# Kernel optimization log

Measured on AMD Instinct MI355X. Metric: run time of the kernel, lower is better.

The kernel has to match this reference:

```python
import jax, jax.numpy as jnp
import numpy as np

B, T_DEC, T_ENC = 64, 128, 256
D_IN, D_ENC, H = 256, 512, 512


def setup_inputs() -> dict:
    key = jax.random.key(0)
    ks = jax.random.split(key, 8)
    s = 0.05  # keras 'uniform' init is small; keep params modest
    return {
        "inputs": jax.random.normal(ks[0], (B, T_DEC, D_IN), jnp.float32),
        "context_mat": jax.random.normal(ks[1], (B, T_ENC, D_ENC), jnp.float32),
        "att_w1": jax.random.uniform(ks[2], (H + D_ENC, D_ENC), jnp.float32, -s, s),
        "att_w2": jax.random.uniform(ks[3], (D_ENC, 1), jnp.float32, -s, s),
        "Wx": jax.random.uniform(ks[4], (D_IN + D_ENC, 3 * H), jnp.float32, -s, s),
        "Wh": jax.random.uniform(ks[5], (H, 3 * H), jnp.float32, -s, s),
        "b": jnp.zeros((3 * H,), jnp.float32),
    }


def reference(inputs, context_mat, att_w1, att_w2, Wx, Wh, b):
    # inputs: [B, T_dec, d_in]; context_mat: [B, T_enc, d_enc]
    Bn, Te, De = context_mat.shape
    Hn = Wh.shape[0]

    def step(h, x_t):
        # --- Bahdanau-style attention (concat -> relu(MLP) -> softmax) ---
        key_rep = jnp.broadcast_to(h[:, None, :], (Bn, Te, Hn))
        concated = jnp.concatenate([key_rep, context_mat], axis=-1)  # [B,Te,H+De]
        energies = jax.nn.relu(
            jnp.einsum('bte,eo->bto', concated @ att_w1, att_w2)[..., 0]
        )  # [B, Te]
        att = jax.nn.softmax(energies, axis=-1)
        ctx = jnp.einsum('bt,btd->bd', att, context_mat)  # [B, De]
        # --- GRU cell (reset_after=False, classic Keras) ---
        xin = jnp.concatenate([x_t, ctx], axis=-1)  # [B, d_in+De]
        gx = xin @ Wx + b  # [B, 3H]
        xz, xr, xh = gx[:, :Hn], gx, gx  # slices below
        xz = gx[:, :Hn]
        xr = gx[:, Hn:2 * Hn]
        xh = gx[:, 2 * Hn:]
        z = jax.nn.sigmoid(xz + h @ Wh[:, :Hn])
        r = jax.nn.sigmoid(xr + h @ Wh[:, Hn:2 * Hn])
        hh = jnp.tanh(xh + (r * h) @ Wh[:, 2 * Hn:])
        h_new = z * h + (1.0 - z) * hh
        return h_new, h_new

    h0 = jnp.zeros((Bn, Hn), inputs.dtype)
    xs = jnp.swapaxes(inputs, 0, 1)  # [T_dec, B, d_in]
    _, outs = jax.lax.scan(step, h0, xs)  # [T_dec, B, H]
    return jnp.swapaxes(outs, 0, 1)  # [B, T_dec, H]
```

## Files before the change

kernel.cpp:

```cpp
#include <hip/hip_runtime.h>

#define NBLK  256
#define NTHR  384
#define TDEC  128
#define TENC  256
#define DIN   256
#define DENC  512
#define HHH   512
#define NG    1536
#define KTOT  1280
#define NK4   320
#define ASTR  516
#define ASTR4 129

#define FLAGS_BYTES (128*3*16*16)
#define OFF_U     24576
#define OFF_ECTX  25600
#define OFF_HG    41984
#define OFF_CTXG  74752
#define OFF_RHG   107520
#define OFF_WP    140288
#define WP_ELEMS  (16*NK4*96*4)

__device__ __forceinline__ float wave_sum(float v) {
#pragma unroll
    for (int o = 32; o; o >>= 1) v += __shfl_down(v, o, 64);
    return v;
}
__device__ __forceinline__ float wave_max(float v) {
#pragma unroll
    for (int o = 32; o; o >>= 1) v = fmaxf(v, __shfl_down(v, o, 64));
    return v;
}
__device__ __forceinline__ void stA(float* p, float v) {
    __hip_atomic_store(p, v, __ATOMIC_RELAXED, __HIP_MEMORY_SCOPE_AGENT);
}
__device__ __forceinline__ float2 ldA2(float* p) {
    double d = __hip_atomic_load((double*)p, __ATOMIC_RELAXED, __HIP_MEMORY_SCOPE_AGENT);
    return *(float2*)&d;
}
__device__ __forceinline__ void drain_stores() {
    asm volatile("s_waitcnt vmcnt(0)" ::: "memory");
}
__device__ __forceinline__ void setflag(unsigned char* p) {
    __hip_atomic_store(p, (unsigned char)1, __ATOMIC_RELAXED, __HIP_MEMORY_SCOPE_AGENT);
}
__device__ __forceinline__ void waitflags16(unsigned* f) {
    for (;;) {
        unsigned a0 = __hip_atomic_load(f + 0, __ATOMIC_RELAXED, __HIP_MEMORY_SCOPE_AGENT);
        unsigned a1 = __hip_atomic_load(f + 1, __ATOMIC_RELAXED, __HIP_MEMORY_SCOPE_AGENT);
        unsigned a2 = __hip_atomic_load(f + 2, __ATOMIC_RELAXED, __HIP_MEMORY_SCOPE_AGENT);
        unsigned a3 = __hip_atomic_load(f + 3, __ATOMIC_RELAXED, __HIP_MEMORY_SCOPE_AGENT);
        if ((a0 & a1 & a2 & a3) == 0x01010101u) return;
        __builtin_amdgcn_s_sleep(2);
    }
}
__device__ __forceinline__ float blo(unsigned u) { return __uint_as_float(u << 16); }
__device__ __forceinline__ float bhi(unsigned u) { return __uint_as_float(u & 0xffff0000u); }
__device__ __forceinline__ unsigned short f2bf(float f) {
    unsigned u = __float_as_uint(f);
    u += 0x7fffu + ((u >> 16) & 1u);
    return (unsigned short)(u >> 16);
}

template<bool BF>
__device__ __forceinline__ float4 dotq(const void* wp, int cg, int kcol,
                                       int k4lo, int k4hi, const float* abase,
                                       int aoff, float4 acc) {
    if (BF) {
        const uint2* w = (const uint2*)wp + (size_t)cg*NK4*96 + kcol;
#pragma unroll 4
        for (int k4 = k4lo; k4 < k4hi; ++k4) {
            uint2 uu = w[(size_t)k4 * 96];
            float wx = blo(uu.x), wy = bhi(uu.x), wz = blo(uu.y), ww = bhi(uu.y);
            const float* ao = abase + (k4 - aoff)*4;
            float4 A0 = *(const float4*)(ao + 0*ASTR);
            float4 A1 = *(const float4*)(ao + 1*ASTR);
            float4 A2 = *(const float4*)(ao + 2*ASTR);
            float4 A3 = *(const float4*)(ao + 3*ASTR);
            acc.x = fmaf(wx, A0.x, acc.x); acc.x = fmaf(wy, A0.y, acc.x);
            acc.x = fmaf(wz, A0.z, acc.x); acc.x = fmaf(ww, A0.w, acc.x);
            acc.y = fmaf(wx, A1.x, acc.y); acc.y = fmaf(wy, A1.y, acc.y);
            acc.y = fmaf(wz, A1.z, acc.y); acc.y = fmaf(ww, A1.w, acc.y);
            acc.z = fmaf(wx, A2.x, acc.z); acc.z = fmaf(wy, A2.y, acc.z);
            acc.z = fmaf(wz, A2.z, acc.z); acc.z = fmaf(ww, A2.w, acc.z);
            acc.w = fmaf(wx, A3.x, acc.w); acc.w = fmaf(wy, A3.y, acc.w);
            acc.w = fmaf(wz, A3.z, acc.w); acc.w = fmaf(ww, A3.w, acc.w);
        }
    } else {
        const float4* w = (const float4*)wp + (size_t)cg*NK4*96 + kcol;
#pragma unroll 4
        for (int k4 = k4lo; k4 < k4hi; ++k4) {
            float4 wv = w[(size_t)k4 * 96];
            const float* ao = abase + (k4 - aoff)*4;
            float4 A0 = *(const float4*)(ao + 0*ASTR);
            float4 A1 = *(const float4*)(ao + 1*ASTR);
            float4 A2 = *(const float4*)(ao + 2*ASTR);
            float4 A3 = *(const float4*)(ao + 3*ASTR);
            acc.x = fmaf(wv.x, A0.x, acc.x); acc.x = fmaf(wv.y, A0.y, acc.x);
            acc.x = fmaf(wv.z, A0.z, acc.x); acc.x = fmaf(wv.w, A0.w, acc.x);
            acc.y = fmaf(wv.x, A1.x, acc.y); acc.y = fmaf(wv.y, A1.y, acc.y);
            acc.y = fmaf(wv.z, A1.z, acc.y); acc.y = fmaf(wv.w, A1.w, acc.y);
            acc.z = fmaf(wv.x, A2.x, acc.z); acc.z = fmaf(wv.y, A2.y, acc.z);
            acc.z = fmaf(wv.z, A2.z, acc.z); acc.z = fmaf(wv.w, A2.w, acc.z);
            acc.w = fmaf(wv.x, A3.x, acc.w); acc.w = fmaf(wv.y, A3.y, acc.w);
            acc.w = fmaf(wv.z, A3.z, acc.w); acc.w = fmaf(wv.w, A3.w, acc.w);
        }
    }
    return acc;
}

__global__ void k_u(const float* __restrict__ w1, const float* __restrict__ w2,
                    float* __restrict__ u) {
    int e = blockIdx.x;
    int lane = threadIdx.x;
    float p = 0.f;
#pragma unroll
    for (int k = lane; k < DENC; k += 64) p += w1[e*DENC + k] * w2[k];
    p = wave_sum(p);
    if (lane == 0) u[e] = p;
}

__global__ void k_ectx(const float* __restrict__ C, const float* __restrict__ u,
                       float* __restrict__ ectx) {
    int r = blockIdx.x*4 + (threadIdx.x >> 6);
    int lane = threadIdx.x & 63;
    const float* row = C + (size_t)r*DENC;
    const float* vc  = u + HHH;
    float p = 0.f;
#pragma unroll
    for (int k = 0; k < DENC/64; ++k) p += row[lane + k*64] * vc[lane + k*64];
    p = wave_sum(p);
    if (lane == 0) ectx[r] = p;
}

template<bool BF>
__global__ void k_wpack(const float* __restrict__ Wx, const float* __restrict__ Wh,
                        void* __restrict__ wp) {
    int id = blockIdx.x*256 + threadIdx.x;
    int e = id & 3;
    int q = id >> 2;
    int col = q % 96;
    q /= 96;
    int k4 = q % NK4;
    int cg = q / NK4;
    int k = k4*4 + e;
    int j = (col >> 5)*512 + cg*32 + (col & 31);
    float v = (k < 768) ? Wx[(size_t)k*NG + j] : Wh[(size_t)(k-768)*NG + j];
    if (BF) ((unsigned short*)wp)[id] = f2bf(v);
    else    ((float*)wp)[id] = v;
}

template<bool BF>
__launch_bounds__(NTHR, 1)
__global__ void decoder(const float* __restrict__ inp, const float* __restrict__ C,
                        const float* __restrict__ bias, const void* __restrict__ wpv,
                        const float* __restrict__ u, float* __restrict__ ectx_g,
                        float* __restrict__ out, float* __restrict__ ws) {
    unsigned char* fl = (unsigned char*)ws;
    float* hG   = ws + OFF_HG;
    float* ctxG = ws + OFF_CTXG;
    float* rhG  = ws + OFF_RHG;

    const int tid  = threadIdx.x;
    const int w    = tid >> 6;
    const int blk  = blockIdx.x;
    const int bg   = blk >> 4;
    const int cg   = blk & 15;
    const int b_att = blk >> 2;
    const int ds    = blk & 3;
    const int bl_att = b_att & 3;
    const int ks   = tid / 96;
    const int kcol = tid - ks*96;
    const int sub  = kcol >> 5;
    const int q32k = kcol & 31;
    const int jpk  = cg*32 + q32k;

    __shared__ float sh_C[TENC*128];
    __shared__ __align__(16) float sh_st[4*ASTR];
    __shared__ __align__(16) float sh_h[4*ASTR];
    __shared__ __align__(16) float sh_part[1536];
    __shared__ float sh_att[TENC];
    __shared__ float sh_ectx[TENC];
    __shared__ __align__(16) float sh_u[512];
    __shared__ float sh_z[128];
    __shared__ float sh_cred[2][128];
    __shared__ float sh_red[4];
    __shared__ float sh_hdp[2];

    const float4* u4 = (const float4*)sh_u;

    for (int i = tid; i < TENC*128; i += NTHR)
        sh_C[i] = C[((size_t)b_att*TENC + (i >> 7))*DENC + ds*128 + (i & 127)];
    if (tid < TENC) sh_ectx[tid] = ectx_g[b_att*TENC + tid];
    if (tid < 128) ((float4*)sh_u)[tid] = ((const float4*)(u))[tid];
    const float bias_c = bias[sub*512 + jpk];

    for (int t = 0; t < TDEC; ++t) {
        __syncthreads();
        if (tid < 256) {
            int bb = tid >> 6, k4i = tid & 63;
            *(float4*)&sh_st[bb*ASTR + k4i*4] =
                *(const float4*)&inp[((size_t)(bg*4 + bb)*TDEC + t)*DIN + k4i*4];
        }
        __syncthreads();

        float4 acc = make_float4(ks == 0 ? bias_c : 0.f, ks == 0 ? bias_c : 0.f,
                                 ks == 0 ? bias_c : 0.f, ks == 0 ? bias_c : 0.f);
        acc = dotq<BF>(wpv, cg, kcol, ks*16, ks*16 + 16, sh_st, 0, acc);

        if (t > 0) {
            if (tid == 0) waitflags16((unsigned*)(fl + ((((t-1)*3 + 2)*16 + bg) << 4)));
            __syncthreads();
        }
        if (t > 0) {
            for (int i = tid; i < 1024; i += NTHR) {
                int bb = i >> 8, j2 = (i & 255)*2;
                float2 f = ldA2(&hG[(size_t)(bg*4 + bb)*HHH + j2]);
                *(float2*)&sh_h[bb*ASTR + j2] = f;
            }
        } else {
            for (int i = tid; i < 1024; i += NTHR) {
                int bb = i >> 8, j2 = (i & 255)*2;
                *(float2*)&sh_h[bb*ASTR + j2] = make_float2(0.f, 0.f);
            }
        }
        __syncthreads();

        if (tid < 128) {
            float4 uu = u4[tid];
            float4 hh = ((const float4*)(sh_h + bl_att*ASTR))[tid];
            float p = uu.x*hh.x + uu.y*hh.y + uu.z*hh.z + uu.w*hh.w;
            p = wave_sum(p);
            if ((tid & 63) == 0) sh_hdp[w] = p;
        }
        __syncthreads();
        const float hd = sh_hdp[0] + sh_hdp[1];

        if (tid < TENC) {
            float e = fmaxf(hd + sh_ectx[tid], 0.f);
            float wm = wave_max(e);
            if ((tid & 63) == 0) sh_red[w] = wm;
            __syncthreads();
            float mx = fmaxf(fmaxf(sh_red[0], sh_red[1]), fmaxf(sh_red[2], sh_red[3]));
            float ex = __expf(e - mx);
            float wse = wave_sum(ex);
            __syncthreads();
            if ((tid & 63) == 0) sh_red[w] = wse;
            __syncthreads();
            float dn = sh_red[0] + sh_red[1] + sh_red[2] + sh_red[3];
            sh_att[tid] = ex / dn;
        } else {
            __syncthreads(); __syncthreads(); __syncthreads();
        }
        __syncthreads();

        if (tid < TENC) {
            const int dp = tid & 127, hf = tid >> 7;
            const float* Cl = sh_C + (size_t)hf*128*128 + dp;
            float a = 0.f;
#pragma unroll 8
            for (int q = 0; q < 128; ++q)
                a = fmaf(sh_att[hf*128 + q], Cl[(size_t)q*128], a);
            sh_cred[hf][dp] = a;
        }
        __syncthreads();
        if (tid < 128) stA(&ctxG[(size_t)b_att*HHH + ds*128 + tid],
                           sh_cred[0][tid] + sh_cred[1][tid]);
        drain_stores();
        __syncthreads();
        if (tid == 0) setflag(fl + (((t*3 + 0)*16 + bg) << 4) + cg);

        if (t > 0 && kcol < 64)
            acc = dotq<BF>(wpv, cg, kcol, 192 + ks*32, 192 + ks*32 + 32, sh_h, 192, acc);

        if (tid == 0) waitflags16((unsigned*)(fl + (((t*3 + 0)*16 + bg) << 4)));
        __syncthreads();
        for (int i = tid; i < 1024; i += NTHR) {
            int bb = i >> 8, j2 = (i & 255)*2;
            float2 f = ldA2(&ctxG[(size_t)(bg*4 + bb)*HHH + j2]);
            *(float2*)&sh_st[bb*ASTR + j2] = f;
        }
        __syncthreads();
        acc = dotq<BF>(wpv, cg, kcol, 64 + ks*32, 64 + ks*32 + 32, sh_st, 64, acc);

        __syncthreads();
        if (kcol < 64) *(float4*)&sh_part[tid*4 - ks*384 + ks*384] = acc;
        __syncthreads();
        if (tid < 256) {
            int cz = tid >> 2, b = tid & 3;
            float s = sh_part[0*384 + cz*4 + b] + sh_part[1*384 + cz*4 + b]
                    + sh_part[2*384 + cz*4 + b] + sh_part[3*384 + cz*4 + b];
            if (cz < 32) {
                sh_z[cz*4 + b] = 1.f / (1.f + __expf(-s));
            } else {
                int jp = cg*32 + (cz - 32);
                float r = 1.f / (1.f + __expf(-s));
                stA(&rhG[(size_t)(bg*4 + b)*HHH + jp], r * sh_h[b*ASTR + jp]);
            }
        }
        drain_stores();
        __syncthreads();
        if (tid == 0) setflag(fl + (((t*3 + 1)*16 + bg) << 4) + cg);

        if (tid == 0) waitflags16((unsigned*)(fl + (((t*3 + 1)*16 + bg) << 4)));
        __syncthreads();
        for (int i = tid; i < 1024; i += NTHR) {
            int bb = i >> 8, j2 = (i & 255)*2;
            float2 f = ldA2(&rhG[(size_t)(bg*4 + bb)*HHH + j2]);
            *(float2*)&sh_st[bb*ASTR + j2] = f;
        }
        __syncthreads();
        if (kcol >= 64) {
            acc = dotq<BF>(wpv, cg, kcol, 192 + ks*32, 192 + ks*32 + 32, sh_st, 192, acc);
            *(float4*)&sh_part[(ks*96 + kcol)*4] = acc;
        }
        __syncthreads();
        if (tid < 128) {
            int ch = 64 + (tid >> 2), b = tid & 3;
            float s = sh_part[0*384 + ch*4 + b] + sh_part[1*384 + ch*4 + b]
                    + sh_part[2*384 + ch*4 + b] + sh_part[3*384 + ch*4 + b];
            int q32 = ch - 64;
            int jp = cg*32 + q32;
            float hh = tanhf(s);
            float z  = sh_z[q32*4 + b];
            float hp = sh_h[b*ASTR + jp];
            float hn = z*hp + (1.f - z)*hh;
            stA(&hG[(size_t)(bg*4 + b)*HHH + jp], hn);
            out[((size_t)(bg*4 + b)*TDEC + t)*HHH + jp] = hn;
        }
        drain_stores();
        __syncthreads();
        if (tid == 0) setflag(fl + (((t*3 + 2)*16 + bg) << 4) + cg);
    }
}

extern "C" void kernel_launch(void* const* d_in, const int* in_sizes, int n_in,
                              void* d_out, int out_size, void* d_ws, size_t ws_size,
                              hipStream_t stream) {
    const float* inputs = (const float*)d_in[0];
    const float* C      = (const float*)d_in[1];
    const float* w1     = (const float*)d_in[2];
    const float* w2     = (const float*)d_in[3];
    const float* Wx     = (const float*)d_in[4];
    const float* Wh     = (const float*)d_in[5];
    const float* bias   = (const float*)d_in[6];
    float* out = (float*)d_out;
    float* ws  = (float*)d_ws;

    hipMemsetAsync(ws, 0, FLAGS_BYTES, stream);

    k_u   <<<1024, 64,  0, stream>>>(w1, w2, ws + OFF_U);
    k_ectx<<<(64*TENC)/4, 256, 0, stream>>>(C, ws + OFF_U, ws + OFF_ECTX);

    const size_t need_f32 = (size_t)(OFF_WP) * 4u + (size_t)WP_ELEMS * 4u;
    void* wp = (void*)(ws + OFF_WP);
    if (ws_size >= need_f32) {
        k_wpack<false><<<WP_ELEMS/256, 256, 0, stream>>>(Wx, Wh, wp);
        decoder<false><<<NBLK, NTHR, 0, stream>>>(inputs, C, bias, wp,
                                                  ws + OFF_U, ws + OFF_ECTX, out, ws);
    } else {
        k_wpack<true><<<WP_ELEMS/256, 256, 0, stream>>>(Wx, Wh, wp);
        decoder<true><<<NBLK, NTHR, 0, stream>>>(inputs, C, bias, wp,
                                                 ws + OFF_U, ws + OFF_ECTX, out, ws);
    }
}
```

Baseline: 2.912 ms.

## Publish partial h·u dot products and overlap hidden/context loads with compute

Each block now computes its slice's partial dot of the new hidden state with u and publishes it to a global buffer. At the next step the attention scalar is formed by summing 16 partials, so the full h no longer has to be in shared memory before attention starts. The h and ctx global loads are issued into registers early and written to shared memory later, and the recurrent-weight dot is split in two halves to hide the ctx load latency. The s_sleep in the flag spin loop is also removed, which lowers wake-up latency at the cost of more polling traffic.

```diff
diff --git a/kernel.cpp b/kernel.cpp
--- a/kernel.cpp
+++ b/kernel.cpp
@@ -19,7 +19,8 @@
 #define OFF_HG    41984
 #define OFF_CTXG  74752
 #define OFF_RHG   107520
-#define OFF_WP    140288
+#define OFF_HD    140288
+#define OFF_WP    141312
 #define WP_ELEMS  (16*NK4*96*4)
 
 __device__ __forceinline__ float wave_sum(float v) {
@@ -34,6 +35,9 @@
 }
 __device__ __forceinline__ void stA(float* p, float v) {
     __hip_atomic_store(p, v, __ATOMIC_RELAXED, __HIP_MEMORY_SCOPE_AGENT);
+}
+__device__ __forceinline__ float ldAf(float* p) {
+    return __hip_atomic_load(p, __ATOMIC_RELAXED, __HIP_MEMORY_SCOPE_AGENT);
 }
 __device__ __forceinline__ float2 ldA2(float* p) {
     double d = __hip_atomic_load((double*)p, __ATOMIC_RELAXED, __HIP_MEMORY_SCOPE_AGENT);
@@ -52,7 +56,6 @@
         unsigned a2 = __hip_atomic_load(f + 2, __ATOMIC_RELAXED, __HIP_MEMORY_SCOPE_AGENT);
         unsigned a3 = __hip_atomic_load(f + 3, __ATOMIC_RELAXED, __HIP_MEMORY_SCOPE_AGENT);
         if ((a0 & a1 & a2 & a3) == 0x01010101u) return;
-        __builtin_amdgcn_s_sleep(2);
     }
 }
 __device__ __forceinline__ float blo(unsigned u) { return __uint_as_float(u << 16); }
@@ -161,6 +164,7 @@
     float* hG   = ws + OFF_HG;
     float* ctxG = ws + OFF_CTXG;
     float* rhG  = ws + OFF_RHG;
+    float* hdP  = ws + OFF_HD;
 
     const int tid  = threadIdx.x;
     const int w    = tid >> 6;
@@ -169,7 +173,7 @@
     const int cg   = blk & 15;
     const int b_att = blk >> 2;
     const int ds    = blk & 3;
-    const int bl_att = b_att & 3;
+    const int bl_att = cg >> 2;
     const int ks   = tid / 96;
     const int kcol = tid - ks*96;
     const int sub  = kcol >> 5;
@@ -186,9 +190,8 @@
     __shared__ float sh_z[128];
     __shared__ float sh_cred[2][128];
     __shared__ float sh_red[4];
-    __shared__ float sh_hdp[2];
-
-    const float4* u4 = (const float4*)sh_u;
+    __shared__ float sh_hdp[8];
+    __shared__ float sh_scal;
 
     for (int i = tid; i < TENC*128; i += NTHR)
         sh_C[i] = C[((size_t)b_att*TENC + (i >> 7))*DENC + ds*128 + (i & 127)];
@@ -196,6 +199,8 @@
     if (tid < 128) ((float4*)sh_u)[tid] = ((const float4*)(u))[tid];
     const float bias_c = bias[sub*512 + jpk];
 
+    const int i0 = tid, i1 = tid + 384, i2 = tid + 768;
+
     for (int t = 0; t < TDEC; ++t) {
         __syncthreads();
         if (tid < 256) {
@@ -213,29 +218,27 @@
             if (tid == 0) waitflags16((unsigned*)(fl + ((((t-1)*3 + 2)*16 + bg) << 4)));
             __syncthreads();
         }
+
+        float2 h0, h1, h2;
         if (t > 0) {
-            for (int i = tid; i < 1024; i += NTHR) {
-                int bb = i >> 8, j2 = (i & 255)*2;
-                float2 f = ldA2(&hG[(size_t)(bg*4 + bb)*HHH + j2]);
-                *(float2*)&sh_h[bb*ASTR + j2] = f;
+            h0 = ldA2(&hG[(size_t)(bg*4 + (i0 >> 8))*HHH + (i0 & 255)*2]);
+            h1 = ldA2(&hG[(size_t)(bg*4 + (i1 >> 8))*HHH + (i1 & 255)*2]);
+            if (i2 < 1024)
+                h2 = ldA2(&hG[(size_t)(bg*4 + (i2 >> 8))*HHH + (i2 & 255)*2]);
+        }
+
+        if (t > 0) {
+            if (tid < 64) {
+                float v = (tid < 16) ? ldAf(&hdP[(bg*16 + tid)*4 + bl_att]) : 0.f;
+                v += __shfl_xor(v, 1, 64);
+                v += __shfl_xor(v, 2, 64);
+                v += __shfl_xor(v, 4, 64);
+                v += __shfl_xor(v, 8, 64);
+                if (tid == 0) sh_scal = v;
             }
-        } else {
-            for (int i = tid; i < 1024; i += NTHR) {
-                int bb = i >> 8, j2 = (i & 255)*2;
-                *(float2*)&sh_h[bb*ASTR + j2] = make_float2(0.f, 0.f);
-            }
-        }
-        __syncthreads();
-
-        if (tid < 128) {
-            float4 uu = u4[tid];
-            float4 hh = ((const float4*)(sh_h + bl_att*ASTR))[tid];
-            float p = uu.x*hh.x + uu.y*hh.y + uu.z*hh.z + uu.w*hh.w;
-            p = wave_sum(p);
-            if ((tid & 63) == 0) sh_hdp[w] = p;
-        }
-        __syncthreads();
-        const float hd = sh_hdp[0] + sh_hdp[1];
+        } else if (tid == 0) sh_scal = 0.f;
+        __syncthreads();
+        const float hd = sh_scal;
 
         if (tid < TENC) {
             float e = fmaxf(hd + sh_ectx[tid], 0.f);
@@ -271,21 +274,37 @@
         __syncthreads();
         if (tid == 0) setflag(fl + (((t*3 + 0)*16 + bg) << 4) + cg);
 
+        if (t > 0) {
+            *(float2*)&sh_h[(i0 >> 8)*ASTR + (i0 & 255)*2] = h0;
+            *(float2*)&sh_h[(i1 >> 8)*ASTR + (i1 & 255)*2] = h1;
+            if (i2 < 1024) *(float2*)&sh_h[(i2 >> 8)*ASTR + (i2 & 255)*2] = h2;
+        } else {
+            for (int i = tid; i < 1024; i += NTHR)
+                *(float2*)&sh_h[(i >> 8)*ASTR + (i & 255)*2] = make_float2(0.f, 0.f);
+        }
+        __syncthreads();
+
         if (t > 0 && kcol < 64)
-            acc = dotq<BF>(wpv, cg, kcol, 192 + ks*32, 192 + ks*32 + 32, sh_h, 192, acc);
+            acc = dotq<BF>(wpv, cg, kcol, 192 + ks*32, 192 + ks*32 + 16, sh_h, 192, acc);
 
         if (tid == 0) waitflags16((unsigned*)(fl + (((t*3 + 0)*16 + bg) << 4)));
         __syncthreads();
-        for (int i = tid; i < 1024; i += NTHR) {
-            int bb = i >> 8, j2 = (i & 255)*2;
-            float2 f = ldA2(&ctxG[(size_t)(bg*4 + bb)*HHH + j2]);
-            *(float2*)&sh_st[bb*ASTR + j2] = f;
-        }
-        __syncthreads();
+        float2 c0, c1, c2;
+        c0 = ldA2(&ctxG[(size_t)(bg*4 + (i0 >> 8))*HHH + (i0 & 255)*2]);
+        c1 = ldA2(&ctxG[(size_t)(bg*4 + (i1 >> 8))*HHH + (i1 & 255)*2]);
+        if (i2 < 1024)
+            c2 = ldA2(&ctxG[(size_t)(bg*4 + (i2 >> 8))*HHH + (i2 & 255)*2]);
+        if (t > 0 && kcol < 64)
+            acc = dotq<BF>(wpv, cg, kcol, 192 + ks*32 + 16, 192 + ks*32 + 32, sh_h, 192, acc);
+        *(float2*)&sh_st[(i0 >> 8)*ASTR + (i0 & 255)*2] = c0;
+        *(float2*)&sh_st[(i1 >> 8)*ASTR + (i1 & 255)*2] = c1;
+        if (i2 < 1024) *(float2*)&sh_st[(i2 >> 8)*ASTR + (i2 & 255)*2] = c2;
+        __syncthreads();
+
         acc = dotq<BF>(wpv, cg, kcol, 64 + ks*32, 64 + ks*32 + 32, sh_st, 64, acc);
 
         __syncthreads();
-        if (kcol < 64) *(float4*)&sh_part[tid*4 - ks*384 + ks*384] = acc;
+        if (kcol < 64) *(float4*)&sh_part[tid*4] = acc;
         __syncthreads();
         if (tid < 256) {
             int cz = tid >> 2, b = tid & 3;
@@ -317,10 +336,10 @@
         }
         __syncthreads();
         if (tid < 128) {
-            int ch = 64 + (tid >> 2), b = tid & 3;
+            int q32 = tid >> 2, b = tid & 3;
+            int ch = 64 + q32;
             float s = sh_part[0*384 + ch*4 + b] + sh_part[1*384 + ch*4 + b]
                     + sh_part[2*384 + ch*4 + b] + sh_part[3*384 + ch*4 + b];
-            int q32 = ch - 64;
             int jp = cg*32 + q32;
             float hh = tanhf(s);
             float z  = sh_z[q32*4 + b];
@@ -328,7 +347,15 @@
             float hn = z*hp + (1.f - z)*hh;
             stA(&hG[(size_t)(bg*4 + b)*HHH + jp], hn);
             out[((size_t)(bg*4 + b)*TDEC + t)*HHH + jp] = hn;
-        }
+            float p = sh_u[jp] * hn;
+            p += __shfl_xor(p, 4, 64);
+            p += __shfl_xor(p, 8, 64);
+            p += __shfl_xor(p, 16, 64);
+            p += __shfl_xor(p, 32, 64);
+            if ((tid & 63) < 4) sh_hdp[(tid >> 6)*4 + (tid & 3)] = p;
+        }
+        __syncthreads();
+        if (tid < 4) stA(&hdP[(bg*16 + cg)*4 + tid], sh_hdp[tid] + sh_hdp[4 + tid]);
         drain_stores();
         __syncthreads();
         if (tid == 0) setflag(fl + (((t*3 + 2)*16 + bg) << 4) + cg);
```

After: 3.376 ms. 1.16x slower.
